# Kernel optimization log

Hardware: AMD Instinct MI355X
Metric: run time of the kernel (lower is better)

## Reference

```python
import jax, jax.numpy as jnp
import numpy as np

B, S, E, H = 2, 2048, 1024, 16
DH = E // H


def setup_inputs() -> dict:
    key = jax.random.key(0)
    ks = jax.random.split(key, 8)
    scale = 1.0 / np.sqrt(E)
    return {
        "in_feats": jax.random.normal(ks[0], (B, S, E), jnp.float32),
        "mul_encs": jax.random.normal(ks[1], (B, S, E), jnp.float32),
        "add_encs": jax.random.normal(ks[2], (B, S, E), jnp.float32),
        "ln_w": jnp.ones((E,), jnp.float32),
        "ln_b": jnp.zeros((E,), jnp.float32),
        "in_proj_w": jax.random.uniform(ks[3], (3 * E, E), jnp.float32, -scale, scale),
        "in_proj_b": jnp.zeros((3 * E,), jnp.float32),
        "out_proj_w": jax.random.uniform(ks[4], (E, E), jnp.float32, -scale, scale),
        "out_proj_b": jnp.zeros((E,), jnp.float32),
    }


def _layernorm(x, w, b, eps=1e-5):
    mu = jnp.mean(x, axis=-1, keepdims=True)
    var = jnp.var(x, axis=-1, keepdims=True)
    return (x - mu) * jax.lax.rsqrt(var + eps) * w + b


def reference(in_feats, mul_encs, add_encs, ln_w, ln_b, in_proj_w, in_proj_b, out_proj_w, out_proj_b):
    # norm + act pre-processing (torch nn.GELU default = exact erf gelu)
    d = _layernorm(in_feats, ln_w, ln_b)
    d = jax.nn.gelu(d, approximate=False)
    values = d
    qk_in = d * mul_encs + add_encs  # QK encoding modulation

    wq, wk, wv = jnp.split(in_proj_w, 3, axis=0)
    bq, bk, bv = jnp.split(in_proj_b, 3, axis=0)
    q = (qk_in @ wq.T + bq).reshape(B, S, H, DH)
    k = (qk_in @ wk.T + bk).reshape(B, S, H, DH)
    v = (values @ wv.T + bv).reshape(B, S, H, DH)

    scale = 1.0 / np.sqrt(DH)
    scores = jnp.einsum("bqhd,bkhd->bhqk", q * scale, k)  # [B,H,S,S]
    attn = jax.nn.softmax(scores, axis=-1)
    out = jnp.einsum("bhqk,bkhd->bqhd", attn, v).reshape(B, S, E)
    out = out @ out_proj_w.T + out_proj_b
    return in_feats + out  # skip connection
```

## Files before the change

### kernel.cpp

```cpp
#include <hip/hip_runtime.h>
#include <stdint.h>


typedef __attribute__((ext_vector_type(8))) short bf16x8;
typedef __attribute__((ext_vector_type(4))) short bf16x4;
typedef __attribute__((ext_vector_type(4))) float f32x4;
typedef __attribute__((ext_vector_type(4))) unsigned short u16x4;

#define DEV __device__ __forceinline__

DEV unsigned short f2bf(float f) {
  uint32_t u = __float_as_uint(f);
  u += 0x7fff + ((u >> 16) & 1);
  return (unsigned short)(u >> 16);
}

DEV float fast_exp2(float x) {
#if __has_builtin(__builtin_amdgcn_exp2f)
  return __builtin_amdgcn_exp2f(x);
#else
  return exp2f(x);
#endif
}

DEV f32x4 mfma16x16x16_bf16(bf16x4 a, bf16x4 b, f32x4 c) {
#if __has_builtin(__builtin_amdgcn_mfma_f32_16x16x16bf16_1k)
  return __builtin_amdgcn_mfma_f32_16x16x16bf16_1k(a, b, c, 0, 0, 0);
#else
  asm("v_mfma_f32_16x16x16_bf16 %0, %1, %2, %0" : "+v"(c) : "v"(a), "v"(b));
  return c;
#endif
}

DEV void gload_lds16(const void* g, void* l) {
  __builtin_amdgcn_global_load_lds(
      (const __attribute__((address_space(1))) uint32_t*)g,
      (__attribute__((address_space(3))) uint32_t*)l, 16, 0, 0);
}

__global__ __launch_bounds__(256) void preproc_wconv(const float* x, const float* mul, const float* add,
                                                     const float* lw, const float* lb,
                                                     unsigned short* values, unsigned short* qkin,
                                                     const float* w1, const float* w2,
                                                     unsigned short* o1, unsigned short* o2) {
  int t = threadIdx.x;
  if (blockIdx.x >= 4096) {
    int i = (blockIdx.x - 4096) * 256 + t;
    const int n1 = 3145728 / 4;
    f32x4 v;
    if (i < n1) v = ((const f32x4*)w1)[i];
    else        v = ((const f32x4*)w2)[i - n1];
    u16x4 r;
#pragma unroll
    for (int j = 0; j < 4; ++j) r[j] = f2bf(v[j]);
    if (i < n1) ((u16x4*)o1)[i] = r;
    else        ((u16x4*)o2)[i - n1] = r;
    return;
  }
  int row = blockIdx.x;
  size_t base = (size_t)row * 1024;
  f32x4 v = ((const f32x4*)(x + base))[t];
  float s  = v[0] + v[1] + v[2] + v[3];
  float s2 = v[0]*v[0] + v[1]*v[1] + v[2]*v[2] + v[3]*v[3];
#pragma unroll
  for (int off = 1; off < 64; off <<= 1) {
    s  += __shfl_xor(s, off);
    s2 += __shfl_xor(s2, off);
  }
  __shared__ float rs[4], rs2[4];
  if ((t & 63) == 0) { rs[t >> 6] = s; rs2[t >> 6] = s2; }
  __syncthreads();
  s  = rs[0] + rs[1] + rs[2] + rs[3];
  s2 = rs2[0] + rs2[1] + rs2[2] + rs2[3];
  float mean = s * 0.0009765625f;
  float var  = s2 * 0.0009765625f - mean * mean;
  float rstd = rsqrtf(var + 1e-5f);
  f32x4 mu = ((const f32x4*)(mul + base))[t];
  f32x4 ad = ((const f32x4*)(add + base))[t];
  f32x4 w4 = ((const f32x4*)lw)[t];
  f32x4 b4 = ((const f32x4*)lb)[t];
  u16x4 vo, qo;
#pragma unroll
  for (int i = 0; i < 4; ++i) {
    float d = (v[i] - mean) * rstd * w4[i] + b4[i];
    float g = 0.5f * d * (1.0f + erff(d * 0.70710678118f));
    vo[i] = f2bf(g);
    qo[i] = f2bf(g * mu[i] + ad[i]);
  }
  ((u16x4*)(values + base))[t] = vo;
  ((u16x4*)(qkin   + base))[t] = qo;
}

#define QSCALE 0.18033688011112042f

DEV void qkv_stage(const unsigned short* A, const unsigned short* W,
                   int m0, int n0, int k0, unsigned short* buf, int t) {
  int w = t >> 6;
  unsigned short* ldsA = buf;
  unsigned short* ldsB = buf + 64 * 64;
  {
    int idx = t;
    int r = idx >> 3;
    int slot = (idx & 7) ^ (r & 7);
    gload_lds16(A + (size_t)(m0 + r) * 1024 + k0 + slot * 8,
                (char*)ldsA + w * 1024);
  }
#pragma unroll
  for (int i = 0; i < 2; ++i) {
    int idx = i * 512 + t;
    int r = idx >> 3;
    int slot = (idx & 7) ^ (r & 7);
    gload_lds16(W + (size_t)(n0 + r) * 1024 + k0 + slot * 8,
                (char*)ldsB + i * 8192 + w * 1024);
  }
}

__global__ __launch_bounds__(512) void gemm_qkv(const unsigned short* Aqk, const unsigned short* Av,
                                                const unsigned short* W, const float* bias,
                                                unsigned short* qws, unsigned short* kws,
                                                unsigned short* vtws) {
  __shared__ unsigned short lds[2][(64 + 128) * 64];
  int id = blockIdx.x;
  int xcd = id & 7, rr = id >> 3;
  int bx = xcd * 3 + (rr % 3);
  int by = rr / 3;
  int n0 = bx * 128;
  int m0 = by * 64;
  const unsigned short* A = (n0 < 2048) ? Aqk : Av;
  int t = threadIdx.x, lane = t & 63, w = t >> 6;
  int wr = w & 3, wc = w >> 2;
  int l15 = lane & 15, l4 = lane >> 4;
  f32x4 z = {0.f, 0.f, 0.f, 0.f};
  f32x4 acc[4];
#pragma unroll
  for (int nn = 0; nn < 4; ++nn) acc[nn] = z;

  qkv_stage(A, W, m0, n0, 0, &lds[0][0], t);
  __syncthreads();

  for (int it = 0; it < 16; ++it) {
    int cur = it & 1;
    if (it < 15) qkv_stage(A, W, m0, n0, (it + 1) * 64, &lds[cur ^ 1][0], t);
    const unsigned short* ldsA = &lds[cur][0];
    const unsigned short* ldsB = &lds[cur][64 * 64];
#pragma unroll
    for (int kk = 0; kk < 2; ++kk) {
      bf16x8 af, bfr[4];
      int kb = kk * 64 + l4 * 16;
      {
        int r = wr * 16 + l15;
        af = *(const bf16x8*)((const char*)ldsA + r * 128 + (kb ^ ((r & 7) << 4)));
      }
#pragma unroll
      for (int nn = 0; nn < 4; ++nn) {
        int r = wc * 64 + nn * 16 + l15;
        bfr[nn] = *(const bf16x8*)((const char*)ldsB + r * 128 + (kb ^ ((r & 7) << 4)));
      }
#pragma unroll
      for (int nn = 0; nn < 4; ++nn)
        acc[nn] = __builtin_amdgcn_mfma_f32_16x16x32_bf16(af, bfr[nn], acc[nn], 0, 0, 0);
    }
    __syncthreads();
  }

  int region = n0 >> 10;
  int bb = m0 >> 11, s0 = m0 & 2047;

  if (region == 2) {
    unsigned short* sc = &lds[0][0];
#pragma unroll
    for (int nn = 0; nn < 4; ++nn) {
      int col = wc * 64 + nn * 16 + l15;
      float bs = bias[n0 + col];
#pragma unroll
      for (int reg = 0; reg < 4; ++reg) {
        int row = wr * 16 + l4 * 4 + reg;
        *(unsigned short*)((char*)sc + row * 256 + ((col * 2) ^ ((row & 7) << 4))) =
            f2bf(acc[nn][reg] + bs);
      }
    }
    __syncthreads();
    int c = t >> 2, ql = t & 3;
    int e0 = n0 - 2048;
    int h = (e0 + c) >> 6, d = (e0 + c) & 63;
    unsigned short* dst = vtws + ((size_t)(bb * 16 + h) * 64 + d) * 2048 + s0 + ql * 16;
#pragma unroll
    for (int j0 = 0; j0 < 16; j0 += 8) {
      bf16x8 pk;
#pragma unroll
      for (int j = 0; j < 8; ++j) {
        int s = ql * 16 + j0 + j;
        pk[j] = *(const short*)((const char*)sc + s * 256 + ((c * 2) ^ ((s & 7) << 4)));
      }
      *(bf16x8*)(dst + j0) = pk;
    }
  } else {
    unsigned short* dst0 = region == 0 ? qws : kws;
    float scl = region == 0 ? QSCALE : 1.0f;
    int row0 = m0 + wr * 16 + l4 * 4;
    int sr = row0 & 2047;
#pragma unroll
    for (int nn = 0; nn < 4; ++nn) {
      int col = n0 + wc * 64 + nn * 16 + l15;
      float bs = bias[col];
      int e = col & 1023;
      int h = e >> 6, d = e & 63;
#pragma unroll
      for (int reg = 0; reg < 4; ++reg)
        dst0[(((size_t)(bb * 16 + h)) * 2048 + sr + reg) * 64 + d] = f2bf((acc[nn][reg] + bs) * scl);
    }
  }
}

DEV void stage_k(const unsigned short* Kp, int kv0, unsigned short* buf, int t) {
  int w = t >> 6;
#pragma unroll
  for (int i = 0; i < 2; ++i) {
    int idx = i * 256 + t;
    int r = idx >> 3;
    int slot = (idx & 7) ^ (r & 7);
    gload_lds16(Kp + (size_t)(kv0 + r) * 64 + slot * 8,
                (char*)buf + i * 4096 + w * 1024);
  }
}

DEV void stage_vt(const unsigned short* Vt, int kv0, unsigned short* buf, int t) {
  int w = t >> 6;
#pragma unroll
  for (int i = 0; i < 2; ++i) {
    int idx = i * 256 + t;
    int r = idx >> 3;
    int slot = (idx & 7) ^ (r & 7);
    gload_lds16(Vt + (size_t)r * 2048 + kv0 + slot * 8,
                (char*)buf + i * 4096 + w * 1024);
  }
}

DEV void attn_compute(const unsigned short* kbuf, const unsigned short* vtbuf,
                      const bf16x8 (&aq)[2][2], f32x4 (&o)[2][4],
                      float (&m_run)[2], f32x4 (&l_run4)[2], const int (&osrc)[4],
                      int l15, int l4) {
  const bf16x4 ones4 = {(short)0x3F80, (short)0x3F80, (short)0x3F80, (short)0x3F80};
  f32x4 z = {0.f, 0.f, 0.f, 0.f};
  f32x4 sc[2][4];
#pragma unroll
  for (int qs = 0; qs < 2; ++qs)
#pragma unroll
    for (int nn = 0; nn < 4; ++nn) sc[qs][nn] = z;
  __builtin_amdgcn_s_setprio(1);
#pragma unroll
  for (int kk = 0; kk < 2; ++kk) {
#pragma unroll
    for (int nn = 0; nn < 4; ++nn) {
      int r = nn * 16 + l15;
      bf16x8 bk = *(const bf16x8*)((const char*)kbuf + r * 128 + ((kk * 64 + l4 * 16) ^ ((r & 7) << 4)));
#pragma unroll
      for (int qs = 0; qs < 2; ++qs)
        sc[qs][nn] = __builtin_amdgcn_mfma_f32_16x16x32_bf16(bk, aq[qs][kk], sc[qs][nn], 0, 0, 0);
    }
  }
  __builtin_amdgcn_s_setprio(0);

  bf16x4 pa[2][4];
  float pmax[2];
#pragma unroll
  for (int qs = 0; qs < 2; ++qs) {
    float mA = fmaxf(fmaxf(sc[qs][0][0], sc[qs][0][1]), fmaxf(sc[qs][0][2], sc[qs][0][3]));
    float mB = fmaxf(fmaxf(sc[qs][1][0], sc[qs][1][1]), fmaxf(sc[qs][1][2], sc[qs][1][3]));
    float mC = fmaxf(fmaxf(sc[qs][2][0], sc[qs][2][1]), fmaxf(sc[qs][2][2], sc[qs][2][3]));
    float mD = fmaxf(fmaxf(sc[qs][3][0], sc[qs][3][1]), fmaxf(sc[qs][3][2], sc[qs][3][3]));
    float pm = fmaxf(fmaxf(mA, mB), fmaxf(mC, mD));
    pm = fmaxf(pm, __shfl_xor(pm, 16));
    pm = fmaxf(pm, __shfl_xor(pm, 32));
    pmax[qs] = pm;
  }

  if (__any(fmaxf(pmax[0] - m_run[0], pmax[1] - m_run[1]) > 8.0f)) {
#pragma unroll
    for (int qs = 0; qs < 2; ++qs) {
      float mnew = fmaxf(m_run[qs], pmax[qs]);
      float fs = fast_exp2(m_run[qs] - mnew);
      m_run[qs] = mnew;
      float fo[4];
#pragma unroll
      for (int reg = 0; reg < 4; ++reg) fo[reg] = __shfl(fs, osrc[reg]);
#pragma unroll
      for (int reg = 0; reg < 4; ++reg) l_run4[qs][reg] *= fo[reg];
#pragma unroll
      for (int dt = 0; dt < 4; ++dt)
#pragma unroll
        for (int reg = 0; reg < 4; ++reg) o[qs][dt][reg] *= fo[reg];
    }
  }

#pragma unroll
  for (int qs = 0; qs < 2; ++qs) {
#pragma unroll
    for (int nn = 0; nn < 4; ++nn) {
      float p0 = fast_exp2(sc[qs][nn][0] - m_run[qs]);
      float p1 = fast_exp2(sc[qs][nn][1] - m_run[qs]);
      float p2 = fast_exp2(sc[qs][nn][2] - m_run[qs]);
      float p3 = fast_exp2(sc[qs][nn][3] - m_run[qs]);
      pa[qs][nn][0] = (short)(__float_as_uint(p0) >> 16);
      pa[qs][nn][1] = (short)(__float_as_uint(p1) >> 16);
      pa[qs][nn][2] = (short)(__float_as_uint(p2) >> 16);
      pa[qs][nn][3] = (short)(__float_as_uint(p3) >> 16);
    }
  }

  __builtin_amdgcn_s_setprio(1);
#pragma unroll
  for (int nn = 0; nn < 4; ++nn)
#pragma unroll
    for (int qs = 0; qs < 2; ++qs)
      l_run4[qs] = mfma16x16x16_bf16(pa[qs][nn], ones4, l_run4[qs]);
#pragma unroll
  for (int dt = 0; dt < 4; ++dt) {
    int r = dt * 16 + l15;
#pragma unroll
    for (int nn = 0; nn < 4; ++nn) {
      bf16x4 vb = *(const bf16x4*)((const char*)vtbuf + r * 128 + ((nn * 32 + l4 * 8) ^ ((r & 7) << 4)));
#pragma unroll
      for (int qs = 0; qs < 2; ++qs)
        o[qs][dt] = mfma16x16x16_bf16(pa[qs][nn], vb, o[qs][dt]);
    }
  }
  __builtin_amdgcn_s_setprio(0);
}

__global__ __launch_bounds__(256, 4) void attn_kernel(const unsigned short* qws, const unsigned short* kws,
                                                      const unsigned short* vtws,
                                                      unsigned short* po0, unsigned short* po1,
                                                      float* stats) {
  int id = blockIdx.x;
  int xcd = id & 7, rr = id >> 3;
  int c = xcd * 8 + (rr & 7);
  int qt = rr >> 3;
  int bh = c & 31;
  int half = c >> 5;
  int q0 = qt * 128;
  int kvbase = half * 1024;
  int t = threadIdx.x;
  int lane = t & 63, w = t >> 6;
  int l15 = lane & 15, l4 = lane >> 4;
  __shared__ unsigned short ldsK[2][64 * 64];
  __shared__ unsigned short ldsVT[2][64 * 64];

  const unsigned short* Qp = qws + ((size_t)bh * 2048 + q0 + w * 32) * 64;
  const unsigned short* Kp = kws + ((size_t)bh * 2048 + kvbase) * 64;
  const unsigned short* Vt = vtws + (size_t)bh * 64 * 2048 + kvbase;

  bf16x8 aq[2][2];
#pragma unroll
  for (int qs = 0; qs < 2; ++qs)
#pragma unroll
    for (int kk = 0; kk < 2; ++kk)
      aq[qs][kk] = *(const bf16x8*)(Qp + (qs * 16 + l15) * 64 + kk * 32 + l4 * 8);

  f32x4 z = {0.f, 0.f, 0.f, 0.f};
  f32x4 o[2][4];
#pragma unroll
  for (int qs = 0; qs < 2; ++qs)
#pragma unroll
    for (int i = 0; i < 4; ++i) o[qs][i] = z;
  float m_run[2] = {-1e30f, -1e30f};
  f32x4 l_run4[2] = {z, z};

  int osrc[4];
#pragma unroll
  for (int reg = 0; reg < 4; ++reg)
    osrc[reg] = (lane & 48) | (((lane >> 4) & 3) << 2) | reg;

  stage_k(Kp, 0, &ldsK[0][0], t);
  stage_vt(Vt, 0, &ldsVT[0][0], t);
  __syncthreads();

  for (int it = 0; it < 16; ++it) {
    int cur = it & 1;
    if (it < 15) {
      stage_k(Kp, (it + 1) * 64, &ldsK[cur ^ 1][0], t);
      stage_vt(Vt, (it + 1) * 64, &ldsVT[cur ^ 1][0], t);
    }
    attn_compute(&ldsK[cur][0], &ldsVT[cur][0], aq, o, m_run, l_run4, osrc, l15, l4);
    __syncthreads();
  }

  unsigned short* po = half ? po1 : po0;
#pragma unroll
  for (int qs = 0; qs < 2; ++qs) {
#pragma unroll
    for (int reg = 0; reg < 4; ++reg) {
      int qg = q0 + w * 32 + qs * 16 + l4 * 4 + reg;
#pragma unroll
      for (int dt = 0; dt < 4; ++dt) {
        int d = dt * 16 + l15;
        po[((size_t)bh * 2048 + qg) * 64 + d] = f2bf(o[qs][dt][reg]);
      }
    }
  }
  if (l4 == 0) {
#pragma unroll
    for (int qs = 0; qs < 2; ++qs) {
      int qg = q0 + w * 32 + qs * 16 + l15;
      size_t si = (((size_t)half * 32 + bh) * 2048 + qg) * 2;
      stats[si] = m_run[qs];
    }
  }
  if (l15 == 0) {
#pragma unroll
    for (int qs = 0; qs < 2; ++qs) {
#pragma unroll
      for (int reg = 0; reg < 4; ++reg) {
        int qg = q0 + w * 32 + qs * 16 + l4 * 4 + reg;
        size_t si = (((size_t)half * 32 + bh) * 2048 + qg) * 2;
        stats[si + 1] = l_run4[qs][reg];
      }
    }
  }
}

__global__ __launch_bounds__(256) void attn_merge(const unsigned short* po0, const unsigned short* po1,
                                                  const float* stats, unsigned short* attnb) {
  int row = blockIdx.x;
  int b = row >> 11, q = row & 2047;
  int t = threadIdx.x;
  int c0 = t * 4;
  int h = c0 >> 6, d = c0 & 63;
  int bh = b * 16 + h;
  size_t si0 = ((size_t)bh * 2048 + q) * 2;
  size_t si1 = (((size_t)32 + bh) * 2048 + q) * 2;
  float m0 = stats[si0], l0 = stats[si0 + 1];
  float m1 = stats[si1], l1 = stats[si1 + 1];
  float m = fmaxf(m0, m1);
  float f0 = fast_exp2(m0 - m), f1 = fast_exp2(m1 - m);
  float inv = 1.0f / (l0 * f0 + l1 * f1);
  float a0 = f0 * inv, a1 = f1 * inv;
  size_t off = ((size_t)bh * 2048 + q) * 64 + d;
  u16x4 x0 = *(const u16x4*)(po0 + off);
  u16x4 x1 = *(const u16x4*)(po1 + off);
  u16x4 r;
#pragma unroll
  for (int j = 0; j < 4; ++j) {
    float v0 = __uint_as_float((uint32_t)x0[j] << 16);
    float v1 = __uint_as_float((uint32_t)x1[j] << 16);
    r[j] = f2bf(v0 * a0 + v1 * a1);
  }
  *(u16x4*)(attnb + (size_t)row * 1024 + c0) = r;
}

__global__ __launch_bounds__(256) void gemm_out(const unsigned short* A, const unsigned short* W,
                                                const float* bias, const float* resid, float* out) {
  __shared__ unsigned short ldsA[64 * 64];
  __shared__ unsigned short ldsB[64 * 64];
  int id = blockIdx.x;
  int xcd = id & 7, rr = id >> 3;
  int bx = xcd * 2 + (rr & 1);
  int by = rr >> 1;
  int n0 = bx * 64;
  int m0 = by * 64;
  int t = threadIdx.x;
  int lane = t & 63;
  int w = t >> 6;
  int l15 = lane & 15, l4 = lane >> 4;
  f32x4 z = {0.f, 0.f, 0.f, 0.f};
  f32x4 acc[4];
#pragma unroll
  for (int nn = 0; nn < 4; ++nn) acc[nn] = z;

  for (int k0 = 0; k0 < 1024; k0 += 64) {
#pragma unroll
    for (int i = 0; i < 2; ++i) {
      int idx = i * 256 + t;
      int r = idx >> 3;
      int slot = (idx & 7) ^ (r & 7);
      gload_lds16(A + (size_t)(m0 + r) * 1024 + k0 + slot * 8,
                  (char*)ldsA + i * 4096 + w * 1024);
    }
#pragma unroll
    for (int i = 0; i < 2; ++i) {
      int idx = i * 256 + t;
      int r = idx >> 3;
      int slot = (idx & 7) ^ (r & 7);
      gload_lds16(W + (size_t)(n0 + r) * 1024 + k0 + slot * 8,
                  (char*)ldsB + i * 4096 + w * 1024);
    }
    __syncthreads();
#pragma unroll
    for (int kk = 0; kk < 2; ++kk) {
      bf16x8 af, bfr[4];
      int kb = kk * 64 + l4 * 16;
      {
        int r = w * 16 + l15;
        af = *(const bf16x8*)((const char*)ldsA + r * 128 + (kb ^ ((r & 7) << 4)));
      }
#pragma unroll
      for (int nn = 0; nn < 4; ++nn) {
        int r = nn * 16 + l15;
        bfr[nn] = *(const bf16x8*)((const char*)ldsB + r * 128 + (kb ^ ((r & 7) << 4)));
      }
#pragma unroll
      for (int nn = 0; nn < 4; ++nn)
        acc[nn] = __builtin_amdgcn_mfma_f32_16x16x32_bf16(af, bfr[nn], acc[nn], 0, 0, 0);
    }
    __syncthreads();
  }

#pragma unroll
  for (int nn = 0; nn < 4; ++nn) {
    int col = n0 + nn * 16 + l15;
    float bs = bias[col];
#pragma unroll
    for (int reg = 0; reg < 4; ++reg) {
      int r = m0 + w * 16 + l4 * 4 + reg;
      size_t off = (size_t)r * 1024 + col;
      out[off] = acc[nn][reg] + bs + resid[off];
    }
  }
}

extern "C" void kernel_launch(void* const* d_in, const int* in_sizes, int n_in,
                              void* d_out, int out_size, void* d_ws, size_t ws_size,
                              hipStream_t stream) {
  const float* in_feats   = (const float*)d_in[0];
  const float* mul_encs   = (const float*)d_in[1];
  const float* add_encs   = (const float*)d_in[2];
  const float* ln_w       = (const float*)d_in[3];
  const float* ln_b       = (const float*)d_in[4];
  const float* in_proj_w  = (const float*)d_in[5];
  const float* in_proj_b  = (const float*)d_in[6];
  const float* out_proj_w = (const float*)d_in[7];
  const float* out_proj_b = (const float*)d_in[8];
  float* out = (float*)d_out;

  unsigned short* ws = (unsigned short*)d_ws;
  unsigned short* values = ws;
  unsigned short* qkin   = values + 4194304;
  unsigned short* wqkv   = qkin + 4194304;
  unsigned short* wout   = wqkv + 3145728;
  unsigned short* qws    = wout + 1048576;
  unsigned short* kws    = qws + 4194304;
  unsigned short* vtws   = kws + 4194304;
  unsigned short* attnb  = vtws + 4194304;

  unsigned short* po0   = values;
  unsigned short* po1   = qkin;
  float*          stats = (float*)wqkv;

  preproc_wconv<<<8192, 256, 0, stream>>>(in_feats, mul_encs, add_encs, ln_w, ln_b,
                                          values, qkin, in_proj_w, out_proj_w, wqkv, wout);
  gemm_qkv<<<1536, 512, 0, stream>>>(qkin, values, wqkv, in_proj_b, qws, kws, vtws);
  attn_kernel<<<1024, 256, 0, stream>>>(qws, kws, vtws, po0, po1, stats);
  attn_merge<<<4096, 256, 0, stream>>>(po0, po1, stats, attnb);
  gemm_out<<<1024, 256, 0, stream>>>(attnb, wout, out_proj_b, in_feats, out);
}
```

Measured before the change: 130.0 us.

## Split attention KV range four ways with smaller KV tiles and higher occupancy

Templates the attention kernel on the KV block size. When the workspace is large enough, the KV range is split into four partitions instead of two, giving 2048 blocks with 32-row KV tiles and a launch bound of 8 blocks per CU. The merge kernel is generalised to combine any number of partial outputs using their max/sum statistics. The aim is more concurrent blocks and better latency hiding per CU. The cost is extra partial-output traffic, a heavier merge and more barriers per KV element; without enough workspace the old two-way path runs instead.

After: 454.3 us. +249.5%, slower.

```diff
diff --git a/kernel.cpp b/kernel.cpp
--- a/kernel.cpp
+++ b/kernel.cpp
@@ -14,6 +14,8 @@
   u += 0x7fff + ((u >> 16) & 1);
   return (unsigned short)(u >> 16);
 }
+
+DEV float bf2f(unsigned short u) { return __uint_as_float((uint32_t)u << 16); }
 
 DEV float fast_exp2(float x) {
 #if __has_builtin(__builtin_amdgcn_exp2f)
@@ -212,10 +214,11 @@
   }
 }
 
-DEV void stage_k(const unsigned short* Kp, int kv0, unsigned short* buf, int t) {
+template<int KVB>
+DEV void stage_kT(const unsigned short* Kp, int kv0, unsigned short* buf, int t) {
   int w = t >> 6;
 #pragma unroll
-  for (int i = 0; i < 2; ++i) {
+  for (int i = 0; i < KVB / 32; ++i) {
     int idx = i * 256 + t;
     int r = idx >> 3;
     int slot = (idx & 7) ^ (r & 7);
@@ -224,34 +227,41 @@
   }
 }
 
-DEV void stage_vt(const unsigned short* Vt, int kv0, unsigned short* buf, int t) {
+template<int KVB>
+DEV void stage_vtT(const unsigned short* Vt, int kv0, unsigned short* buf, int t) {
   int w = t >> 6;
-#pragma unroll
-  for (int i = 0; i < 2; ++i) {
+  constexpr int CPR = KVB / 8;
+#pragma unroll
+  for (int i = 0; i < KVB / 32; ++i) {
     int idx = i * 256 + t;
-    int r = idx >> 3;
-    int slot = (idx & 7) ^ (r & 7);
+    int r = idx / CPR;
+    int g = idx % CPR;
+    int slot = g ^ (r & (CPR - 1));
     gload_lds16(Vt + (size_t)r * 2048 + kv0 + slot * 8,
                 (char*)buf + i * 4096 + w * 1024);
   }
 }
 
-DEV void attn_compute(const unsigned short* kbuf, const unsigned short* vtbuf,
-                      const bf16x8 (&aq)[2][2], f32x4 (&o)[2][4],
-                      float (&m_run)[2], f32x4 (&l_run4)[2], const int (&osrc)[4],
-                      int l15, int l4) {
+template<int KVB>
+DEV void attn_computeT(const unsigned short* kbuf, const unsigned short* vtbuf,
+                       const bf16x8 (&aq)[2][2], f32x4 (&o)[2][4],
+                       float (&m_run)[2], f32x4 (&l_run4)[2], const int (&osrc)[4],
+                       int l15, int l4) {
+  constexpr int NN = KVB / 16;
+  constexpr int RS = KVB * 2;
+  constexpr int VM = (RS >> 4) - 1;
   const bf16x4 ones4 = {(short)0x3F80, (short)0x3F80, (short)0x3F80, (short)0x3F80};
   f32x4 z = {0.f, 0.f, 0.f, 0.f};
-  f32x4 sc[2][4];
+  f32x4 sc[2][NN];
 #pragma unroll
   for (int qs = 0; qs < 2; ++qs)
 #pragma unroll
-    for (int nn = 0; nn < 4; ++nn) sc[qs][nn] = z;
+    for (int nn = 0; nn < NN; ++nn) sc[qs][nn] = z;
   __builtin_amdgcn_s_setprio(1);
 #pragma unroll
   for (int kk = 0; kk < 2; ++kk) {
 #pragma unroll
-    for (int nn = 0; nn < 4; ++nn) {
+    for (int nn = 0; nn < NN; ++nn) {
       int r = nn * 16 + l15;
       bf16x8 bk = *(const bf16x8*)((const char*)kbuf + r * 128 + ((kk * 64 + l4 * 16) ^ ((r & 7) << 4)));
 #pragma unroll
@@ -261,15 +271,14 @@
   }
   __builtin_amdgcn_s_setprio(0);
 
-  bf16x4 pa[2][4];
+  bf16x4 pa[2][NN];
   float pmax[2];
 #pragma unroll
   for (int qs = 0; qs < 2; ++qs) {
-    float mA = fmaxf(fmaxf(sc[qs][0][0], sc[qs][0][1]), fmaxf(sc[qs][0][2], sc[qs][0][3]));
-    float mB = fmaxf(fmaxf(sc[qs][1][0], sc[qs][1][1]), fmaxf(sc[qs][1][2], sc[qs][1][3]));
-    float mC = fmaxf(fmaxf(sc[qs][2][0], sc[qs][2][1]), fmaxf(sc[qs][2][2], sc[qs][2][3]));
-    float mD = fmaxf(fmaxf(sc[qs][3][0], sc[qs][3][1]), fmaxf(sc[qs][3][2], sc[qs][3][3]));
-    float pm = fmaxf(fmaxf(mA, mB), fmaxf(mC, mD));
+    float pm = -1e30f;
+#pragma unroll
+    for (int nn = 0; nn < NN; ++nn)
+      pm = fmaxf(pm, fmaxf(fmaxf(sc[qs][nn][0], sc[qs][nn][1]), fmaxf(sc[qs][nn][2], sc[qs][nn][3])));
     pm = fmaxf(pm, __shfl_xor(pm, 16));
     pm = fmaxf(pm, __shfl_xor(pm, 32));
     pmax[qs] = pm;
@@ -296,7 +305,7 @@
 #pragma unroll
   for (int qs = 0; qs < 2; ++qs) {
 #pragma unroll
-    for (int nn = 0; nn < 4; ++nn) {
+    for (int nn = 0; nn < NN; ++nn) {
       float p0 = fast_exp2(sc[qs][nn][0] - m_run[qs]);
       float p1 = fast_exp2(sc[qs][nn][1] - m_run[qs]);
       float p2 = fast_exp2(sc[qs][nn][2] - m_run[qs]);
@@ -310,7 +319,7 @@
 
   __builtin_amdgcn_s_setprio(1);
 #pragma unroll
-  for (int nn = 0; nn < 4; ++nn)
+  for (int nn = 0; nn < NN; ++nn)
 #pragma unroll
     for (int qs = 0; qs < 2; ++qs)
       l_run4[qs] = mfma16x16x16_bf16(pa[qs][nn], ones4, l_run4[qs]);
@@ -318,8 +327,8 @@
   for (int dt = 0; dt < 4; ++dt) {
     int r = dt * 16 + l15;
 #pragma unroll
-    for (int nn = 0; nn < 4; ++nn) {
-      bf16x4 vb = *(const bf16x4*)((const char*)vtbuf + r * 128 + ((nn * 32 + l4 * 8) ^ ((r & 7) << 4)));
+    for (int nn = 0; nn < NN; ++nn) {
+      bf16x4 vb = *(const bf16x4*)((const char*)vtbuf + r * RS + ((nn * 32 + l4 * 8) ^ ((r & VM) << 4)));
 #pragma unroll
       for (int qs = 0; qs < 2; ++qs)
         o[qs][dt] = mfma16x16x16_bf16(pa[qs][nn], vb, o[qs][dt]);
@@ -328,23 +337,26 @@
   __builtin_amdgcn_s_setprio(0);
 }
 
-__global__ __launch_bounds__(256, 4) void attn_kernel(const unsigned short* qws, const unsigned short* kws,
-                                                      const unsigned short* vtws,
-                                                      unsigned short* po0, unsigned short* po1,
-                                                      float* stats) {
+template<int KVB>
+__global__ __launch_bounds__(256, (KVB == 32 ? 8 : 4)) void attn_kernel(
+    const unsigned short* qws, const unsigned short* kws, const unsigned short* vtws,
+    unsigned short* po0, unsigned short* po1, unsigned short* po2, unsigned short* po3,
+    float* stats, int nsplit) {
+  __shared__ unsigned short ldsK[2][KVB * 64];
+  __shared__ unsigned short ldsVT[2][64 * KVB];
+  int kvspan = 2048 / nsplit;
+  int cpx = 4 * nsplit;
   int id = blockIdx.x;
   int xcd = id & 7, rr = id >> 3;
-  int c = xcd * 8 + (rr & 7);
-  int qt = rr >> 3;
+  int c = xcd * cpx + (rr % cpx);
+  int qt = rr / cpx;
   int bh = c & 31;
-  int half = c >> 5;
+  int qq = c >> 5;
   int q0 = qt * 128;
-  int kvbase = half * 1024;
+  int kvbase = qq * kvspan;
   int t = threadIdx.x;
   int lane = t & 63, w = t >> 6;
   int l15 = lane & 15, l4 = lane >> 4;
-  __shared__ unsigned short ldsK[2][64 * 64];
-  __shared__ unsigned short ldsVT[2][64 * 64];
 
   const unsigned short* Qp = qws + ((size_t)bh * 2048 + q0 + w * 32) * 64;
   const unsigned short* Kp = kws + ((size_t)bh * 2048 + kvbase) * 64;
@@ -371,21 +383,22 @@
   for (int reg = 0; reg < 4; ++reg)
     osrc[reg] = (lane & 48) | (((lane >> 4) & 3) << 2) | reg;
 
-  stage_k(Kp, 0, &ldsK[0][0], t);
-  stage_vt(Vt, 0, &ldsVT[0][0], t);
+  stage_kT<KVB>(Kp, 0, &ldsK[0][0], t);
+  stage_vtT<KVB>(Vt, 0, &ldsVT[0][0], t);
   __syncthreads();
 
-  for (int it = 0; it < 16; ++it) {
+  int iters = kvspan / KVB;
+  for (int it = 0; it < iters; ++it) {
     int cur = it & 1;
-    if (it < 15) {
-      stage_k(Kp, (it + 1) * 64, &ldsK[cur ^ 1][0], t);
-      stage_vt(Vt, (it + 1) * 64, &ldsVT[cur ^ 1][0], t);
-    }
-    attn_compute(&ldsK[cur][0], &ldsVT[cur][0], aq, o, m_run, l_run4, osrc, l15, l4);
+    if (it < iters - 1) {
+      stage_kT<KVB>(Kp, (it + 1) * KVB, &ldsK[cur ^ 1][0], t);
+      stage_vtT<KVB>(Vt, (it + 1) * KVB, &ldsVT[cur ^ 1][0], t);
+    }
+    attn_computeT<KVB>(&ldsK[cur][0], &ldsVT[cur][0], aq, o, m_run, l_run4, osrc, l15, l4);
     __syncthreads();
   }
 
-  unsigned short* po = half ? po1 : po0;
+  unsigned short* po = qq == 0 ? po0 : (qq == 1 ? po1 : (qq == 2 ? po2 : po3));
 #pragma unroll
   for (int qs = 0; qs < 2; ++qs) {
 #pragma unroll
@@ -402,7 +415,7 @@
 #pragma unroll
     for (int qs = 0; qs < 2; ++qs) {
       int qg = q0 + w * 32 + qs * 16 + l15;
-      size_t si = (((size_t)half * 32 + bh) * 2048 + qg) * 2;
+      size_t si = (((size_t)qq * 32 + bh) * 2048 + qg) * 2;
       stats[si] = m_run[qs];
     }
   }
@@ -412,14 +425,16 @@
 #pragma unroll
       for (int reg = 0; reg < 4; ++reg) {
         int qg = q0 + w * 32 + qs * 16 + l4 * 4 + reg;
-        size_t si = (((size_t)half * 32 + bh) * 2048 + qg) * 2;
+        size_t si = (((size_t)qq * 32 + bh) * 2048 + qg) * 2;
         stats[si + 1] = l_run4[qs][reg];
       }
     }
   }
 }
 
+template<int NSPLIT>
 __global__ __launch_bounds__(256) void attn_merge(const unsigned short* po0, const unsigned short* po1,
+                                                  const unsigned short* po2, const unsigned short* po3,
                                                   const float* stats, unsigned short* attnb) {
   int row = blockIdx.x;
   int b = row >> 11, q = row & 2047;
@@ -427,24 +442,37 @@
   int c0 = t * 4;
   int h = c0 >> 6, d = c0 & 63;
   int bh = b * 16 + h;
-  size_t si0 = ((size_t)bh * 2048 + q) * 2;
-  size_t si1 = (((size_t)32 + bh) * 2048 + q) * 2;
-  float m0 = stats[si0], l0 = stats[si0 + 1];
-  float m1 = stats[si1], l1 = stats[si1 + 1];
-  float m = fmaxf(m0, m1);
-  float f0 = fast_exp2(m0 - m), f1 = fast_exp2(m1 - m);
-  float inv = 1.0f / (l0 * f0 + l1 * f1);
-  float a0 = f0 * inv, a1 = f1 * inv;
+  float ms[NSPLIT], ls[NSPLIT];
+  float m = -1e30f;
+#pragma unroll
+  for (int s = 0; s < NSPLIT; ++s) {
+    size_t si = (((size_t)s * 32 + bh) * 2048 + q) * 2;
+    ms[s] = stats[si];
+    ls[s] = stats[si + 1];
+    m = fmaxf(m, ms[s]);
+  }
+  float a[NSPLIT];
+  float denom = 0.f;
+#pragma unroll
+  for (int s = 0; s < NSPLIT; ++s) {
+    a[s] = fast_exp2(ms[s] - m);
+    denom += ls[s] * a[s];
+  }
+  float inv = 1.0f / denom;
+#pragma unroll
+  for (int s = 0; s < NSPLIT; ++s) a[s] *= inv;
   size_t off = ((size_t)bh * 2048 + q) * 64 + d;
-  u16x4 x0 = *(const u16x4*)(po0 + off);
-  u16x4 x1 = *(const u16x4*)(po1 + off);
+  const unsigned short* pos[4] = {po0, po1, po2, po3};
+  float acc[4] = {0.f, 0.f, 0.f, 0.f};
+#pragma unroll
+  for (int s = 0; s < NSPLIT; ++s) {
+    u16x4 x = *(const u16x4*)(pos[s] + off);
+#pragma unroll
+    for (int j = 0; j < 4; ++j) acc[j] += bf2f((unsigned short)x[j]) * a[s];
+  }
   u16x4 r;
 #pragma unroll
-  for (int j = 0; j < 4; ++j) {
-    float v0 = __uint_as_float((uint32_t)x0[j] << 16);
-    float v1 = __uint_as_float((uint32_t)x1[j] << 16);
-    r[j] = f2bf(v0 * a0 + v1 * a1);
-  }
+  for (int j = 0; j < 4; ++j) r[j] = f2bf(acc[j]);
   *(u16x4*)(attnb + (size_t)row * 1024 + c0) = r;
 }
 
@@ -546,10 +574,19 @@
   unsigned short* po1   = qkin;
   float*          stats = (float*)wqkv;
 
+  bool four = ws_size >= 75497472ull;
+  unsigned short* po2 = four ? (attnb + 4194304) : po0;
+  unsigned short* po3 = four ? (attnb + 8388608) : po1;
+
   preproc_wconv<<<8192, 256, 0, stream>>>(in_feats, mul_encs, add_encs, ln_w, ln_b,
                                           values, qkin, in_proj_w, out_proj_w, wqkv, wout);
   gemm_qkv<<<1536, 512, 0, stream>>>(qkin, values, wqkv, in_proj_b, qws, kws, vtws);
-  attn_kernel<<<1024, 256, 0, stream>>>(qws, kws, vtws, po0, po1, stats);
-  attn_merge<<<4096, 256, 0, stream>>>(po0, po1, stats, attnb);
+  if (four) {
+    attn_kernel<32><<<2048, 256, 0, stream>>>(qws, kws, vtws, po0, po1, po2, po3, stats, 4);
+    attn_merge<4><<<4096, 256, 0, stream>>>(po0, po1, po2, po3, stats, attnb);
+  } else {
+    attn_kernel<64><<<1024, 256, 0, stream>>>(qws, kws, vtws, po0, po1, po2, po3, stats, 2);
+    attn_merge<2><<<4096, 256, 0, stream>>>(po0, po1, po2, po3, stats, attnb);
+  }
   gemm_out<<<1024, 256, 0, stream>>>(attnb, wout, out_proj_b, in_feats, out);
 }
```
